# Performance work log

Measured on AMD Instinct MI355X. Metric: run time of the kernel, lower is better.

The kernel has to match this reference:

```python
import jax, jax.numpy as jnp
import numpy as np

RSD = 9   # robot_state_dim
HSD = 5   # human_state_dim (human feature slice width = HSD+1 = 6)
XD = 32   # X_dim
NEG = -9e15


def _lin(x, w, b):
    return x @ w + b


def _gat(X, adj, w0, b0, w1, b1):
    # X: [B,N,F]; pairwise concat feature (i,j) = [X_i, X_j] -> [B,N,N,2F]
    B, N, F = X.shape
    Xi = jnp.broadcast_to(X[:, :, None, :], (B, N, N, F))
    Xj = jnp.broadcast_to(X[:, None, :, :], (B, N, N, F))
    pair = jnp.concatenate([Xi, Xj], axis=-1)              # [B,N,N,2F]
    h = jax.nn.relu(_lin(pair, w0, b0))                    # [B,N,N,2F]
    A = _lin(h, w1, b1)[..., 0]                            # [B,N,N]
    e = jnp.where(A > 0, A, 0.04 * A)                      # LeakyReLU(0.04)
    att = jax.nn.softmax(jnp.where(adj > 0, e, NEG), axis=2)
    return jnp.einsum('bij,bjf->bif', att, X)


def setup_inputs() -> dict:
    key = jax.random.key(0)
    ks = jax.random.split(key, 32)
    s = 0.05
    d = {
        'state': jax.random.normal(ks[0], (512, 50, 15), jnp.float32),
        'dropout': 0,
        # w_r: Linear(9,64) ReLU Linear(64,32) ReLU
        'wr_w0': jax.random.normal(ks[1], (RSD, 64)) * s, 'wr_b0': jnp.zeros((64,)),
        'wr_w1': jax.random.normal(ks[2], (64, XD)) * s, 'wr_b1': jnp.zeros((XD,)),
        # w_h: Linear(6,64) ReLU Linear(64,32) ReLU
        'wh_w0': jax.random.normal(ks[3], (HSD + 1, 64)) * s, 'wh_b0': jnp.zeros((64,)),
        'wh_w1': jax.random.normal(ks[4], (64, XD)) * s, 'wh_b1': jnp.zeros((XD,)),
        # gat0 w_a: Linear(64,64) ReLU Linear(64,1)
        'g0_w0': jax.random.normal(ks[5], (2 * XD, 2 * XD)) * s, 'g0_b0': jnp.zeros((2 * XD,)),
        'g0_w1': jax.random.normal(ks[6], (2 * XD, 1)) * s, 'g0_b1': jnp.zeros((1,)),
        # gat1 w_a
        'g1_w0': jax.random.normal(ks[7], (2 * XD, 2 * XD)) * s, 'g1_b0': jnp.zeros((2 * XD,)),
        'g1_w1': jax.random.normal(ks[8], (2 * XD, 1)) * s, 'g1_b1': jnp.zeros((1,)),
        # value_net: Linear(32,150) ReLU Linear(150,100) ReLU Linear(100,1) ReLU
        'v_w0': jax.random.normal(ks[9], (XD, 150)) * s, 'v_b0': jnp.zeros((150,)),
        'v_w1': jax.random.normal(ks[10], (150, 100)) * s, 'v_b1': jnp.zeros((100,)),
        'v_w2': jax.random.normal(ks[11], (100, 1)) * s, 'v_b2': jnp.zeros((1,)),
    }
    return d


def reference(state, dropout, wr_w0, wr_b0, wr_w1, wr_b1, wh_w0, wh_b0, wh_w1, wh_b1,
              g0_w0, g0_b0, g0_w1, g0_b1, g1_w0, g1_b0, g1_w1, g1_b1,
              v_w0, v_b0, v_w1, v_b1, v_w2, v_b2):
    B, N, _ = state.shape
    robot = state[:, 0, :RSD]                               # [B,9]
    humans = state[:, :, RSD:]                              # [B,N,6]
    r_emb = jax.nn.relu(_lin(jax.nn.relu(_lin(robot, wr_w0, wr_b0)), wr_w1, wr_b1))[:, None, :]
    h_emb = jax.nn.relu(_lin(jax.nn.relu(_lin(humans, wh_w0, wh_b0)), wh_w1, wh_b1))
    X = jnp.concatenate([r_emb, h_emb], axis=1)             # [B,N+1,32]
    Num = N + 1
    adj = jnp.ones((Num, Num), state.dtype).at[1:, 0].set(0.0)
    adj = jnp.broadcast_to(adj[None], (B, Num, Num))
    H1 = _gat(X, adj, g0_w0, g0_b0, g0_w1, g0_b1)
    H2 = _gat(H1, adj, g1_w0, g1_b0, g1_w1, g1_b1)
    output = H1 + H2 + X                                    # skip_connection=True
    o = output[:, 0, :]
    o = jax.nn.relu(_lin(o, v_w0, v_b0))
    o = jax.nn.relu(_lin(o, v_w1, v_b1))
    o = jax.nn.relu(_lin(o, v_w2, v_b2))                    # last_relu=True
    return o
```

## Files before the change

kernel.cpp:

```cpp
#include <hip/hip_runtime.h>
#include <hip/hip_bf16.h>


typedef float f4 __attribute__((ext_vector_type(4)));
typedef const float* cfp;

__device__ __forceinline__ f4 fma4(float s, f4 v, f4 a) { return a + s * v; }
__device__ __forceinline__ f4 max4(f4 a, f4 b) {
  f4 r;
#pragma unroll
  for (int i = 0; i < 4; ++i) r[i] = fmaxf(a[i], b[i]);
  return r;
}

#define NN 51
#define HID 64
#define XD 32
#define XS 9
#define ES 52

__global__ __launch_bounds__(256)
void value_net_kernel(cfp state,
                      cfp wr_w0, cfp wr_b0, cfp wr_w1, cfp wr_b1,
                      cfp wh_w0, cfp wh_b0, cfp wh_w1, cfp wh_b1,
                      cfp g0_w0, cfp g0_b0, cfp g0_w1, cfp g0_b1,
                      cfp g1_w0, cfp g1_b0, cfp g1_w1, cfp g1_b1,
                      cfp v_w0, cfp v_b0, cfp v_w1, cfp v_b1,
                      cfp v_w2, cfp v_b2,
                      float* out)
{
  __shared__ f4 sX4[52 * XS];
  __shared__ f4 sH14[52 * XS];
  __shared__ f4 sU4[52 * 17];
  __shared__ f4 sV4[52 * 17];
  __shared__ f4 sWE4[1024];
  __shared__ f4 sB04[16];
  __shared__ f4 sW14[16];
  __shared__ float sRH[64];
  __shared__ float sO[32];
  __shared__ float sM1[152];
  __shared__ float sM2[104];

  float* sX  = (float*)sX4;
  float* sH1 = (float*)sH14;
  float* sE  = (float*)sWE4;
  float* sHH = (float*)sU4;
  const f4* sWh4 = (const f4*)sV4;

  const int tid = threadIdx.x;
  const int b = blockIdx.x;
  cfp st = state + b * 750;

  const float gb0 = g0_b1[0];
  const float gb1 = g1_b1[0];

  {
    const f4* g0w04 = (const f4*)g0_w0;
    for (int i = tid; i < 1024; i += 256) sWE4[i] = g0w04[i];
    const f4* whw14 = (const f4*)wh_w1;
    f4* sWh4w = (f4*)sV4;
    for (int i = tid; i < 512; i += 256) sWh4w[i] = whw14[i];
  }
  if (tid < HID) {
    ((float*)sB04)[tid] = g0_b0[tid];
    ((float*)sW14)[tid] = g0_w1[tid];
    float a = wr_b0[tid];
#pragma unroll
    for (int k = 0; k < 9; ++k) a = fmaf(st[k], wr_w0[k * HID + tid], a);
    sRH[tid] = fmaxf(a, 0.f);
  }
  if (tid < XS) { sX4[51 * XS + tid] = (f4){0,0,0,0}; sH14[51 * XS + tid] = (f4){0,0,0,0}; }
  for (int idx = tid; idx < 50 * HID; idx += 256) {
    int i = idx >> 6, t = idx & 63;
    cfp hp = st + i * 15 + 9;
    float a = wh_b0[t];
#pragma unroll
    for (int k = 0; k < 6; ++k) a = fmaf(hp[k], wh_w0[k * HID + t], a);
    sHH[i * 68 + t] = fmaxf(a, 0.f);
  }
  __syncthreads();

  if (tid < XD) {
    float a = wr_b1[tid];
#pragma unroll 8
    for (int t = 0; t < HID; ++t) a = fmaf(sRH[t], wr_w1[t * XD + tid], a);
    sX[tid] = fmaxf(a, 0.f);
  }
  if (tid < 200) {
    int ip = tid >> 3, fg = tid & 7;
    f4 a0 = { wh_b1[fg * 4 + 0], wh_b1[fg * 4 + 1],
              wh_b1[fg * 4 + 2], wh_b1[fg * 4 + 3] };
    f4 a1 = a0;
    const f4* h0 = sU4 + ip * 17;
    const f4* h1 = sU4 + (ip + 25) * 17;
#pragma unroll 4
    for (int tg = 0; tg < 16; ++tg) {
      f4 ha = h0[tg], hb = h1[tg];
#pragma unroll
      for (int e = 0; e < 4; ++e) {
        f4 w = sWh4[(tg * 4 + e) * 8 + fg];
        a0 = fma4(ha[e], w, a0);
        a1 = fma4(hb[e], w, a1);
      }
    }
    f4 z = {0,0,0,0};
    sX4[(1 + ip) * XS + fg] = max4(a0, z);
    sX4[(26 + ip) * XS + fg] = max4(a1, z);
  }
  __syncthreads();

  if (tid < 208) {
    int ip = tid >> 4, tg = tid & 15;
    f4 au[4] = {{0,0,0,0},{0,0,0,0},{0,0,0,0},{0,0,0,0}};
    f4 av[4] = {{0,0,0,0},{0,0,0,0},{0,0,0,0},{0,0,0,0}};
#pragma unroll 2
    for (int kg = 0; kg < 8; ++kg) {
      f4 x0 = sX4[ip * XS + kg];
      f4 x1 = sX4[(ip + 13) * XS + kg];
      f4 x2 = sX4[(ip + 26) * XS + kg];
      f4 x3 = sX4[(ip + 39) * XS + kg];
#pragma unroll
      for (int e = 0; e < 4; ++e) {
        int k = kg * 4 + e;
        f4 wU = sWE4[k * 16 + tg];
        f4 wV = sWE4[(k + 32) * 16 + tg];
        au[0] = fma4(x0[e], wU, au[0]); av[0] = fma4(x0[e], wV, av[0]);
        au[1] = fma4(x1[e], wU, au[1]); av[1] = fma4(x1[e], wV, av[1]);
        au[2] = fma4(x2[e], wU, au[2]); av[2] = fma4(x2[e], wV, av[2]);
        au[3] = fma4(x3[e], wU, au[3]); av[3] = fma4(x3[e], wV, av[3]);
      }
    }
    f4 b0v = sB04[tg];
#pragma unroll
    for (int r = 0; r < 4; ++r) {
      int row = ip + 13 * r;
      sU4[row * 17 + tg] = au[r] + b0v;
      sV4[row * 17 + tg] = av[r];
    }
  }
  __syncthreads();

  if (tid < 169) {
    int it = tid / 13, jt = tid - (tid / 13) * 13;
    const f4* U0 = sU4 + it * 17;
    const f4* V0 = sV4 + jt * 17;
    f4 acc[4][4] = {};
    const f4 z = {0,0,0,0};
#pragma unroll 2
    for (int g = 0; g < 16; ++g) {
      f4 uu[4] = {U0[g], U0[221 + g], U0[442 + g], U0[663 + g]};
      f4 vv[4] = {V0[g], V0[221 + g], V0[442 + g], V0[663 + g]};
      f4 w = sW14[g];
#pragma unroll
      for (int r = 0; r < 4; ++r)
#pragma unroll
        for (int cc = 0; cc < 4; ++cc)
          acc[r][cc] += max4(uu[r] + vv[cc], z) * w;
    }
#pragma unroll
    for (int r = 0; r < 4; ++r) {
      int i = it + 13 * r;
      if (i < NN) {
#pragma unroll
        for (int cc = 0; cc < 4; ++cc) {
          int j = jt + 13 * cc;
          if (j < NN) {
            f4 A4 = acc[r][cc];
            float A = (A4[0] + A4[1]) + (A4[2] + A4[3]) + gb0;
            float e = A > 0.f ? A : 0.04f * A;
            sE[i * ES + j] = (j == 0 && i > 0) ? -1e30f : e;
          }
        }
      }
    }
  }
  __syncthreads();

  {
    int lane = tid & 63, w = tid >> 6;
    for (int r = w; r < NN; r += 4) {
      float* row = sE + r * ES;
      float e = (lane < NN) ? row[lane] : -3.0e38f;
      float m = e;
#pragma unroll
      for (int o = 32; o; o >>= 1) m = fmaxf(m, __shfl_xor(m, o, 64));
      float p = (lane < NN) ? __expf(e - m) : 0.f;
      float s = p;
#pragma unroll
      for (int o = 32; o; o >>= 1) s += __shfl_xor(s, o, 64);
      if (lane < NN) row[lane] = p / s;
      else if (lane == NN) row[lane] = 0.f;
    }
  }
  __syncthreads();

  if (tid < 104) {
    int ip = tid >> 3, q = tid & 7;
    const f4* a0 = (const f4*)(sE + ip * ES);
    const f4* a1 = (const f4*)(sE + (ip + 13) * ES);
    const f4* a2 = (const f4*)(sE + (ip + 26) * ES);
    const f4* a3 = (const f4*)(sE + (ip + 39) * ES);
    f4 b0 = {0,0,0,0}, b1 = {0,0,0,0}, b2 = {0,0,0,0}, b3 = {0,0,0,0};
    for (int jg = 0; jg < 13; ++jg) {
      f4 t0 = a0[jg], t1 = a1[jg], t2 = a2[jg], t3 = a3[jg];
#pragma unroll
      for (int e = 0; e < 4; ++e) {
        f4 x = sX4[(jg * 4 + e) * XS + q];
        b0 = fma4(t0[e], x, b0);
        b1 = fma4(t1[e], x, b1);
        b2 = fma4(t2[e], x, b2);
        b3 = fma4(t3[e], x, b3);
      }
    }
    sH14[ip * XS + q] = b0;
    sH14[(ip + 13) * XS + q] = b1;
    sH14[(ip + 26) * XS + q] = b2;
    sH14[(ip + 39) * XS + q] = b3;
  } else if (tid < 232) {
    int t = tid - 104;
    const f4* g1w = (const f4*)g1_w0;
#pragma unroll
    for (int i = 0; i < 4; ++i) sU4[t + 128 * i] = g1w[512 + t + 128 * i];
  } else if (tid < 248) {
    sB04[tid - 232] = ((const f4*)g1_b0)[tid - 232];
  } else {
    int t = tid - 248;
    sW14[t] = ((const f4*)g1_w1)[t];
    sW14[t + 8] = ((const f4*)g1_w1)[t + 8];
  }
  __syncthreads();

  if (tid < 208) {
    int jp = tid >> 4, tg = tid & 15;
    f4 av[4] = {{0,0,0,0},{0,0,0,0},{0,0,0,0},{0,0,0,0}};
#pragma unroll 2
    for (int kg = 0; kg < 8; ++kg) {
      f4 h0 = sH14[jp * XS + kg];
      f4 h1 = sH14[(jp + 13) * XS + kg];
      f4 h2 = sH14[(jp + 26) * XS + kg];
      f4 h3 = sH14[(jp + 39) * XS + kg];
#pragma unroll
      for (int e = 0; e < 4; ++e) {
        f4 wV = sU4[(kg * 4 + e) * 16 + tg];
        av[0] = fma4(h0[e], wV, av[0]);
        av[1] = fma4(h1[e], wV, av[1]);
        av[2] = fma4(h2[e], wV, av[2]);
        av[3] = fma4(h3[e], wV, av[3]);
      }
    }
#pragma unroll
    for (int r = 0; r < 4; ++r) sV4[(jp + 13 * r) * 17 + tg] = av[r];
  } else if (tid < 224) {
    int tg = tid - 208;
    const f4* w0g = (const f4*)g1_w0;
    f4 au = {0,0,0,0};
#pragma unroll 2
    for (int kg = 0; kg < 8; ++kg) {
      f4 h = sH14[kg];
#pragma unroll
      for (int e = 0; e < 4; ++e) au = fma4(h[e], w0g[(kg * 4 + e) * 16 + tg], au);
    }
    sU4[512 + tg] = au + sB04[tg];
  }
  __syncthreads();

  if (tid < 64) {
    int j = tid;
    float e = -3.0e38f;
    if (j < NN) {
      f4 acc4 = {0,0,0,0};
#pragma unroll 4
      for (int g = 0; g < 16; ++g) {
        f4 u = sU4[512 + g];
        f4 v = sV4[j * 17 + g];
        f4 w = sW14[g];
        f4 z = {0,0,0,0};
        acc4 += max4(u + v, z) * w;
      }
      float acc = (acc4[0] + acc4[1]) + (acc4[2] + acc4[3]) + gb1;
      e = acc > 0.f ? acc : 0.04f * acc;
    }
    float m = e;
#pragma unroll
    for (int o = 32; o; o >>= 1) m = fmaxf(m, __shfl_xor(m, o, 64));
    float p = (j < NN) ? __expf(e - m) : 0.f;
    float s = p;
#pragma unroll
    for (int o = 32; o; o >>= 1) s += __shfl_xor(s, o, 64);
    if (j < NN) sE[j] = p / s;
  }
  __syncthreads();

  if (tid < XD) {
    float a = 0.f;
    for (int j = 0; j < NN; ++j) a = fmaf(sE[j], sH1[j * 36 + tid], a);
    sO[tid] = a + sH1[tid] + sX[tid];
  }
  __syncthreads();

  if (tid < 150) {
    float a = v_b0[tid];
#pragma unroll 8
    for (int k = 0; k < 32; ++k) a = fmaf(sO[k], v_w0[k * 150 + tid], a);
    sM1[tid] = fmaxf(a, 0.f);
  }
  __syncthreads();
  if (tid < 250) {
    int kp = tid / 50, t2 = tid % 50;
    const float2* w = (const float2*)v_w1;
    float2 acc = {0.f, 0.f};
    for (int k = kp * 30; k < kp * 30 + 30; ++k) {
      float2 ww = w[k * 50 + t2];
      float xv = sM1[k];
      acc.x = fmaf(xv, ww.x, acc.x);
      acc.y = fmaf(xv, ww.y, acc.y);
    }
    ((float2*)(sE + 768 + kp * 100))[t2] = acc;
  }
  __syncthreads();
  if (tid < 100) {
    float a = v_b1[tid];
#pragma unroll
    for (int kp = 0; kp < 5; ++kp) a += sE[768 + kp * 100 + tid];
    sM2[tid] = fmaxf(a, 0.f);
  }
  __syncthreads();
  if (tid < 64) {
    float a = sM2[tid] * v_w2[tid];
    if (tid < 36) a = fmaf(sM2[tid + 64], v_w2[tid + 64], a);
#pragma unroll
    for (int o = 32; o; o >>= 1) a += __shfl_xor(a, o, 64);
    if (tid == 0) out[b] = fmaxf(a + v_b2[0], 0.f);
  }
}

extern "C" void kernel_launch(void* const* d_in, const int* in_sizes, int n_in,
                              void* d_out, int out_size, void* d_ws, size_t ws_size,
                              hipStream_t stream) {
  cfp state = (cfp)d_in[0];
  cfp wr_w0 = (cfp)d_in[2],  cfp_wr_b0 = (cfp)d_in[3];
  cfp wr_w1 = (cfp)d_in[4],  wr_b1 = (cfp)d_in[5];
  cfp wh_w0 = (cfp)d_in[6],  wh_b0 = (cfp)d_in[7];
  cfp wh_w1 = (cfp)d_in[8],  wh_b1 = (cfp)d_in[9];
  cfp g0_w0 = (cfp)d_in[10], g0_b0 = (cfp)d_in[11];
  cfp g0_w1 = (cfp)d_in[12], g0_b1 = (cfp)d_in[13];
  cfp g1_w0 = (cfp)d_in[14], g1_b0 = (cfp)d_in[15];
  cfp g1_w1 = (cfp)d_in[16], g1_b1 = (cfp)d_in[17];
  cfp v_w0  = (cfp)d_in[18], v_b0  = (cfp)d_in[19];
  cfp v_w1  = (cfp)d_in[20], v_b1  = (cfp)d_in[21];
  cfp v_w2  = (cfp)d_in[22], v_b2  = (cfp)d_in[23];
  float* out = (float*)d_out;

  const int B = in_sizes[0] / 750;
  hipLaunchKernelGGL(value_net_kernel, dim3(B), dim3(256), 0, stream,
                     state,
                     wr_w0, cfp_wr_b0, wr_w1, wr_b1,
                     wh_w0, wh_b0, wh_w1, wh_b1,
                     g0_w0, g0_b0, g0_w1, g0_b1,
                     g1_w0, g1_b0, g1_w1, g1_b1,
                     v_w0, v_b0, v_w1, v_b1, v_w2, v_b2,
                     out);
}
```

Measured before the change: 137.3 us.

## Double block to 512 threads and retile GAT phases to 3x3 register tiles

The kernel launches 512 threads per block instead of 256. The pairwise attention score phase is retiled from 13x13 threads with 4x4 register tiles to 17x17 threads with 3x3 tiles, and the U/V projections, aggregation, softmax rows and value-net reduction are spread across more threads. The robot embedding's second layer moves onto otherwise idle threads so one barrier can be dropped. The aim is shorter per-block latency and less serial work per thread. The cost is more waves per block and more idle lanes in some phases, which may reduce how many blocks fit on each CU.

New measurement: 130.6 us. 1.05x faster.

```diff
diff --git a/kernel.cpp b/kernel.cpp
--- a/kernel.cpp
+++ b/kernel.cpp
@@ -19,7 +19,7 @@
 #define XS 9
 #define ES 52
 
-__global__ __launch_bounds__(256)
+__global__ __launch_bounds__(512, 4)
 void value_net_kernel(cfp state,
                       cfp wr_w0, cfp wr_b0, cfp wr_w1, cfp wr_b1,
                       cfp wh_w0, cfp wh_b0, cfp wh_w1, cfp wh_b1,
@@ -56,10 +56,10 @@
 
   {
     const f4* g0w04 = (const f4*)g0_w0;
-    for (int i = tid; i < 1024; i += 256) sWE4[i] = g0w04[i];
+    for (int i = tid; i < 1024; i += 512) sWE4[i] = g0w04[i];
     const f4* whw14 = (const f4*)wh_w1;
     f4* sWh4w = (f4*)sV4;
-    for (int i = tid; i < 512; i += 256) sWh4w[i] = whw14[i];
+    if (tid < 512) sWh4w[tid] = whw14[tid];
   }
   if (tid < HID) {
     ((float*)sB04)[tid] = g0_b0[tid];
@@ -69,8 +69,8 @@
     for (int k = 0; k < 9; ++k) a = fmaf(st[k], wr_w0[k * HID + tid], a);
     sRH[tid] = fmaxf(a, 0.f);
   }
-  if (tid < XS) { sX4[51 * XS + tid] = (f4){0,0,0,0}; sH14[51 * XS + tid] = (f4){0,0,0,0}; }
-  for (int idx = tid; idx < 50 * HID; idx += 256) {
+  if (tid >= 64 && tid < 64 + XS) sX4[51 * XS + (tid - 64)] = (f4){0,0,0,0};
+  for (int idx = tid; idx < 50 * HID; idx += 512) {
     int i = idx >> 6, t = idx & 63;
     cfp hp = st + i * 15 + 9;
     float a = wh_b0[t];
@@ -80,12 +80,6 @@
   }
   __syncthreads();
 
-  if (tid < XD) {
-    float a = wr_b1[tid];
-#pragma unroll 8
-    for (int t = 0; t < HID; ++t) a = fmaf(sRH[t], wr_w1[t * XD + tid], a);
-    sX[tid] = fmaxf(a, 0.f);
-  }
   if (tid < 200) {
     int ip = tid >> 3, fg = tid & 7;
     f4 a0 = { wh_b1[fg * 4 + 0], wh_b1[fg * 4 + 1],
@@ -106,19 +100,24 @@
     f4 z = {0,0,0,0};
     sX4[(1 + ip) * XS + fg] = max4(a0, z);
     sX4[(26 + ip) * XS + fg] = max4(a1, z);
-  }
-  __syncthreads();
-
-  if (tid < 208) {
+  } else if (tid >= 448 && tid < 448 + XD) {
+    int t = tid - 448;
+    float a = wr_b1[t];
+#pragma unroll 8
+    for (int k = 0; k < HID; ++k) a = fmaf(sRH[k], wr_w1[k * XD + t], a);
+    sX[t] = fmaxf(a, 0.f);
+  }
+  __syncthreads();
+
+  if (tid < 272) {
     int ip = tid >> 4, tg = tid & 15;
-    f4 au[4] = {{0,0,0,0},{0,0,0,0},{0,0,0,0},{0,0,0,0}};
-    f4 av[4] = {{0,0,0,0},{0,0,0,0},{0,0,0,0},{0,0,0,0}};
+    f4 au[3] = {{0,0,0,0},{0,0,0,0},{0,0,0,0}};
+    f4 av[3] = {{0,0,0,0},{0,0,0,0},{0,0,0,0}};
 #pragma unroll 2
     for (int kg = 0; kg < 8; ++kg) {
       f4 x0 = sX4[ip * XS + kg];
-      f4 x1 = sX4[(ip + 13) * XS + kg];
-      f4 x2 = sX4[(ip + 26) * XS + kg];
-      f4 x3 = sX4[(ip + 39) * XS + kg];
+      f4 x1 = sX4[(ip + 17) * XS + kg];
+      f4 x2 = sX4[(ip + 34) * XS + kg];
 #pragma unroll
       for (int e = 0; e < 4; ++e) {
         int k = kg * 4 + e;
@@ -127,50 +126,45 @@
         au[0] = fma4(x0[e], wU, au[0]); av[0] = fma4(x0[e], wV, av[0]);
         au[1] = fma4(x1[e], wU, au[1]); av[1] = fma4(x1[e], wV, av[1]);
         au[2] = fma4(x2[e], wU, au[2]); av[2] = fma4(x2[e], wV, av[2]);
-        au[3] = fma4(x3[e], wU, au[3]); av[3] = fma4(x3[e], wV, av[3]);
       }
     }
     f4 b0v = sB04[tg];
 #pragma unroll
-    for (int r = 0; r < 4; ++r) {
-      int row = ip + 13 * r;
+    for (int r = 0; r < 3; ++r) {
+      int row = ip + 17 * r;
       sU4[row * 17 + tg] = au[r] + b0v;
       sV4[row * 17 + tg] = av[r];
     }
   }
   __syncthreads();
 
-  if (tid < 169) {
-    int it = tid / 13, jt = tid - (tid / 13) * 13;
+  if (tid < 289) {
+    int it = tid / 17, jt = tid - (tid / 17) * 17;
     const f4* U0 = sU4 + it * 17;
     const f4* V0 = sV4 + jt * 17;
-    f4 acc[4][4] = {};
+    f4 acc[3][3] = {};
     const f4 z = {0,0,0,0};
-#pragma unroll 2
+#pragma unroll 4
     for (int g = 0; g < 16; ++g) {
-      f4 uu[4] = {U0[g], U0[221 + g], U0[442 + g], U0[663 + g]};
-      f4 vv[4] = {V0[g], V0[221 + g], V0[442 + g], V0[663 + g]};
+      f4 uu[3] = {U0[g], U0[289 + g], U0[578 + g]};
+      f4 vv[3] = {V0[g], V0[289 + g], V0[578 + g]};
       f4 w = sW14[g];
 #pragma unroll
-      for (int r = 0; r < 4; ++r)
-#pragma unroll
-        for (int cc = 0; cc < 4; ++cc)
+      for (int r = 0; r < 3; ++r)
+#pragma unroll
+        for (int cc = 0; cc < 3; ++cc)
           acc[r][cc] += max4(uu[r] + vv[cc], z) * w;
     }
 #pragma unroll
-    for (int r = 0; r < 4; ++r) {
-      int i = it + 13 * r;
-      if (i < NN) {
-#pragma unroll
-        for (int cc = 0; cc < 4; ++cc) {
-          int j = jt + 13 * cc;
-          if (j < NN) {
-            f4 A4 = acc[r][cc];
-            float A = (A4[0] + A4[1]) + (A4[2] + A4[3]) + gb0;
-            float e = A > 0.f ? A : 0.04f * A;
-            sE[i * ES + j] = (j == 0 && i > 0) ? -1e30f : e;
-          }
-        }
+    for (int r = 0; r < 3; ++r) {
+      int i = it + 17 * r;
+#pragma unroll
+      for (int cc = 0; cc < 3; ++cc) {
+        int j = jt + 17 * cc;
+        f4 A4 = acc[r][cc];
+        float A = (A4[0] + A4[1]) + (A4[2] + A4[3]) + gb0;
+        float e = A > 0.f ? A : 0.04f * A;
+        sE[i * ES + j] = (j == 0 && i > 0) ? -1e30f : e;
       }
     }
   }
@@ -178,7 +172,7 @@
 
   {
     int lane = tid & 63, w = tid >> 6;
-    for (int r = w; r < NN; r += 4) {
+    for (int r = w; r < NN; r += 8) {
       float* row = sE + r * ES;
       float e = (lane < NN) ? row[lane] : -3.0e38f;
       float m = e;
@@ -194,64 +188,54 @@
   }
   __syncthreads();
 
-  if (tid < 104) {
+  if (tid < 208) {
     int ip = tid >> 3, q = tid & 7;
     const f4* a0 = (const f4*)(sE + ip * ES);
-    const f4* a1 = (const f4*)(sE + (ip + 13) * ES);
-    const f4* a2 = (const f4*)(sE + (ip + 26) * ES);
-    const f4* a3 = (const f4*)(sE + (ip + 39) * ES);
-    f4 b0 = {0,0,0,0}, b1 = {0,0,0,0}, b2 = {0,0,0,0}, b3 = {0,0,0,0};
+    const f4* a1 = (const f4*)(sE + (ip + 26) * ES);
+    f4 b0 = {0,0,0,0}, b1 = {0,0,0,0};
     for (int jg = 0; jg < 13; ++jg) {
-      f4 t0 = a0[jg], t1 = a1[jg], t2 = a2[jg], t3 = a3[jg];
+      f4 t0 = a0[jg], t1 = a1[jg];
 #pragma unroll
       for (int e = 0; e < 4; ++e) {
         f4 x = sX4[(jg * 4 + e) * XS + q];
         b0 = fma4(t0[e], x, b0);
         b1 = fma4(t1[e], x, b1);
-        b2 = fma4(t2[e], x, b2);
-        b3 = fma4(t3[e], x, b3);
       }
     }
     sH14[ip * XS + q] = b0;
-    sH14[(ip + 13) * XS + q] = b1;
-    sH14[(ip + 26) * XS + q] = b2;
-    sH14[(ip + 39) * XS + q] = b3;
-  } else if (tid < 232) {
-    int t = tid - 104;
+    sH14[(ip + 26) * XS + q] = b1;
+  } else if (tid >= 384) {
+    int t = tid - 384;
     const f4* g1w = (const f4*)g1_w0;
 #pragma unroll
     for (int i = 0; i < 4; ++i) sU4[t + 128 * i] = g1w[512 + t + 128 * i];
-  } else if (tid < 248) {
-    sB04[tid - 232] = ((const f4*)g1_b0)[tid - 232];
-  } else {
-    int t = tid - 248;
-    sW14[t] = ((const f4*)g1_w1)[t];
-    sW14[t + 8] = ((const f4*)g1_w1)[t + 8];
-  }
-  __syncthreads();
-
-  if (tid < 208) {
+  } else if (tid >= 352 && tid < 368) {
+    sB04[tid - 352] = ((const f4*)g1_b0)[tid - 352];
+  } else if (tid >= 368 && tid < 384) {
+    sW14[tid - 368] = ((const f4*)g1_w1)[tid - 368];
+  }
+  __syncthreads();
+
+  if (tid < 272) {
     int jp = tid >> 4, tg = tid & 15;
-    f4 av[4] = {{0,0,0,0},{0,0,0,0},{0,0,0,0},{0,0,0,0}};
+    f4 av[3] = {{0,0,0,0},{0,0,0,0},{0,0,0,0}};
 #pragma unroll 2
     for (int kg = 0; kg < 8; ++kg) {
       f4 h0 = sH14[jp * XS + kg];
-      f4 h1 = sH14[(jp + 13) * XS + kg];
-      f4 h2 = sH14[(jp + 26) * XS + kg];
-      f4 h3 = sH14[(jp + 39) * XS + kg];
+      f4 h1 = sH14[(jp + 17) * XS + kg];
+      f4 h2 = sH14[(jp + 34) * XS + kg];
 #pragma unroll
       for (int e = 0; e < 4; ++e) {
         f4 wV = sU4[(kg * 4 + e) * 16 + tg];
         av[0] = fma4(h0[e], wV, av[0]);
         av[1] = fma4(h1[e], wV, av[1]);
         av[2] = fma4(h2[e], wV, av[2]);
-        av[3] = fma4(h3[e], wV, av[3]);
-      }
-    }
-#pragma unroll
-    for (int r = 0; r < 4; ++r) sV4[(jp + 13 * r) * 17 + tg] = av[r];
-  } else if (tid < 224) {
-    int tg = tid - 208;
+      }
+    }
+#pragma unroll
+    for (int r = 0; r < 3; ++r) sV4[(jp + 17 * r) * 17 + tg] = av[r];
+  } else if (tid < 288) {
+    int tg = tid - 272;
     const f4* w0g = (const f4*)g1_w0;
     f4 au = {0,0,0,0};
 #pragma unroll 2
@@ -305,11 +289,11 @@
     sM1[tid] = fmaxf(a, 0.f);
   }
   __syncthreads();
-  if (tid < 250) {
+  if (tid < 500) {
     int kp = tid / 50, t2 = tid % 50;
     const float2* w = (const float2*)v_w1;
     float2 acc = {0.f, 0.f};
-    for (int k = kp * 30; k < kp * 30 + 30; ++k) {
+    for (int k = kp * 15; k < kp * 15 + 15; ++k) {
       float2 ww = w[k * 50 + t2];
       float xv = sM1[k];
       acc.x = fmaf(xv, ww.x, acc.x);
@@ -321,7 +305,7 @@
   if (tid < 100) {
     float a = v_b1[tid];
 #pragma unroll
-    for (int kp = 0; kp < 5; ++kp) a += sE[768 + kp * 100 + tid];
+    for (int kp = 0; kp < 10; ++kp) a += sE[768 + kp * 100 + tid];
     sM2[tid] = fmaxf(a, 0.f);
   }
   __syncthreads();
@@ -338,7 +322,7 @@
                               void* d_out, int out_size, void* d_ws, size_t ws_size,
                               hipStream_t stream) {
   cfp state = (cfp)d_in[0];
-  cfp wr_w0 = (cfp)d_in[2],  cfp_wr_b0 = (cfp)d_in[3];
+  cfp wr_w0 = (cfp)d_in[2],  wr_b0 = (cfp)d_in[3];
   cfp wr_w1 = (cfp)d_in[4],  wr_b1 = (cfp)d_in[5];
   cfp wh_w0 = (cfp)d_in[6],  wh_b0 = (cfp)d_in[7];
   cfp wh_w1 = (cfp)d_in[8],  wh_b1 = (cfp)d_in[9];
@@ -352,9 +336,9 @@
   float* out = (float*)d_out;
 
   const int B = in_sizes[0] / 750;
-  hipLaunchKernelGGL(value_net_kernel, dim3(B), dim3(256), 0, stream,
+  hipLaunchKernelGGL(value_net_kernel, dim3(B), dim3(512), 0, stream,
                      state,
-                     wr_w0, cfp_wr_b0, wr_w1, wr_b1,
+                     wr_w0, wr_b0, wr_w1, wr_b1,
                      wh_w0, wh_b0, wh_w1, wh_b1,
                      g0_w0, g0_b0, g0_w1, g0_b1,
                      g1_w0, g1_b0, g1_w1, g1_b1,
```

## Double block size to 512 threads and redistribute per-stage work across threads

Applied to the files above, without the earlier changes.

Launches 512 threads per batch block instead of 256 and reassigns stage work across the larger thread set. The human-embedding stage now has fewer threads each computing four rows, the robot embedding runs on otherwise idle threads, and the softmax rows and value-net partial sums are spread over more warps. The final softmax and the aggregation are merged into one phase, and the value-net hidden reduction is folded into the last dot product, which removes two barriers. Risks include more idle threads per barrier, higher per-block register and occupancy pressure from the launch bounds, and reading g0_w1 from global memory inside the pairwise loop.

Result: faster. 130.5 us (-5.0%).

```diff
diff --git a/kernel.cpp b/kernel.cpp
--- a/kernel.cpp
+++ b/kernel.cpp
@@ -19,7 +19,7 @@
 #define XS 9
 #define ES 52
 
-__global__ __launch_bounds__(256)
+__global__ __launch_bounds__(512, 4)
 void value_net_kernel(cfp state,
                       cfp wr_w0, cfp wr_b0, cfp wr_w1, cfp wr_b1,
                       cfp wh_w0, cfp wh_b0, cfp wh_w1, cfp wh_b1,
@@ -39,7 +39,6 @@
   __shared__ float sRH[64];
   __shared__ float sO[32];
   __shared__ float sM1[152];
-  __shared__ float sM2[104];
 
   float* sX  = (float*)sX4;
   float* sH1 = (float*)sH14;
@@ -56,21 +55,21 @@
 
   {
     const f4* g0w04 = (const f4*)g0_w0;
-    for (int i = tid; i < 1024; i += 256) sWE4[i] = g0w04[i];
+    for (int i = tid; i < 1024; i += 512) sWE4[i] = g0w04[i];
     const f4* whw14 = (const f4*)wh_w1;
     f4* sWh4w = (f4*)sV4;
-    for (int i = tid; i < 512; i += 256) sWh4w[i] = whw14[i];
+    if (tid < 512) sWh4w[tid] = whw14[tid];
   }
   if (tid < HID) {
     ((float*)sB04)[tid] = g0_b0[tid];
-    ((float*)sW14)[tid] = g0_w1[tid];
     float a = wr_b0[tid];
 #pragma unroll
     for (int k = 0; k < 9; ++k) a = fmaf(st[k], wr_w0[k * HID + tid], a);
     sRH[tid] = fmaxf(a, 0.f);
   }
-  if (tid < XS) { sX4[51 * XS + tid] = (f4){0,0,0,0}; sH14[51 * XS + tid] = (f4){0,0,0,0}; }
-  for (int idx = tid; idx < 50 * HID; idx += 256) {
+  if (tid >= 64 && tid < 64 + XS) sX4[51 * XS + (tid - 64)] = (f4){0,0,0,0};
+  if (tid >= 96 && tid < 130) sU4[850 + (tid - 96)] = (f4){0,0,0,0};
+  for (int idx = tid; idx < 50 * HID; idx += 512) {
     int i = idx >> 6, t = idx & 63;
     cfp hp = st + i * 15 + 9;
     float a = wh_b0[t];
@@ -80,32 +79,37 @@
   }
   __syncthreads();
 
-  if (tid < XD) {
-    float a = wr_b1[tid];
-#pragma unroll 8
-    for (int t = 0; t < HID; ++t) a = fmaf(sRH[t], wr_w1[t * XD + tid], a);
-    sX[tid] = fmaxf(a, 0.f);
-  }
-  if (tid < 200) {
+  if (tid < 104) {
     int ip = tid >> 3, fg = tid & 7;
     f4 a0 = { wh_b1[fg * 4 + 0], wh_b1[fg * 4 + 1],
               wh_b1[fg * 4 + 2], wh_b1[fg * 4 + 3] };
-    f4 a1 = a0;
+    f4 a1 = a0, a2 = a0, a3 = a0;
     const f4* h0 = sU4 + ip * 17;
-    const f4* h1 = sU4 + (ip + 25) * 17;
 #pragma unroll 4
     for (int tg = 0; tg < 16; ++tg) {
-      f4 ha = h0[tg], hb = h1[tg];
+      f4 ha = h0[tg], hb = h0[13 * 17 + tg], hc = h0[26 * 17 + tg], hd = h0[39 * 17 + tg];
 #pragma unroll
       for (int e = 0; e < 4; ++e) {
         f4 w = sWh4[(tg * 4 + e) * 8 + fg];
         a0 = fma4(ha[e], w, a0);
         a1 = fma4(hb[e], w, a1);
+        a2 = fma4(hc[e], w, a2);
+        a3 = fma4(hd[e], w, a3);
       }
     }
     f4 z = {0,0,0,0};
-    sX4[(1 + ip) * XS + fg] = max4(a0, z);
-    sX4[(26 + ip) * XS + fg] = max4(a1, z);
+    f4 res[4] = {max4(a0, z), max4(a1, z), max4(a2, z), max4(a3, z)};
+#pragma unroll
+    for (int r = 0; r < 4; ++r) {
+      int hr = ip + 13 * r;
+      if (hr < 50) sX4[(1 + hr) * XS + fg] = res[r];
+    }
+  } else if (tid >= 448 && tid < 448 + XD) {
+    int t = tid - 448;
+    float a = wr_b1[t];
+#pragma unroll 8
+    for (int k = 0; k < HID; ++k) a = fmaf(sRH[k], wr_w1[k * XD + t], a);
+    sX[t] = fmaxf(a, 0.f);
   }
   __syncthreads();
 
@@ -150,7 +154,8 @@
     for (int g = 0; g < 16; ++g) {
       f4 uu[4] = {U0[g], U0[221 + g], U0[442 + g], U0[663 + g]};
       f4 vv[4] = {V0[g], V0[221 + g], V0[442 + g], V0[663 + g]};
-      f4 w = sW14[g];
+      f4 w = { g0_w1[g * 4 + 0], g0_w1[g * 4 + 1],
+               g0_w1[g * 4 + 2], g0_w1[g * 4 + 3] };
 #pragma unroll
       for (int r = 0; r < 4; ++r)
 #pragma unroll
@@ -178,7 +183,7 @@
 
   {
     int lane = tid & 63, w = tid >> 6;
-    for (int r = w; r < NN; r += 4) {
+    for (int r = w; r < NN; r += 8) {
       float* row = sE + r * ES;
       float e = (lane < NN) ? row[lane] : -3.0e38f;
       float m = e;
@@ -216,17 +221,15 @@
     sH14[(ip + 13) * XS + q] = b1;
     sH14[(ip + 26) * XS + q] = b2;
     sH14[(ip + 39) * XS + q] = b3;
-  } else if (tid < 232) {
-    int t = tid - 104;
+  } else if (tid >= 384) {
+    int t = tid - 384;
     const f4* g1w = (const f4*)g1_w0;
 #pragma unroll
     for (int i = 0; i < 4; ++i) sU4[t + 128 * i] = g1w[512 + t + 128 * i];
-  } else if (tid < 248) {
-    sB04[tid - 232] = ((const f4*)g1_b0)[tid - 232];
-  } else {
-    int t = tid - 248;
-    sW14[t] = ((const f4*)g1_w1)[t];
-    sW14[t + 8] = ((const f4*)g1_w1)[t + 8];
+  } else if (tid >= 352 && tid < 368) {
+    sB04[tid - 352] = ((const f4*)g1_b0)[tid - 352];
+  } else if (tid >= 368 && tid < 384) {
+    sW14[tid - 368] = ((const f4*)g1_w1)[tid - 368];
   }
   __syncthreads();
 
@@ -250,8 +253,8 @@
     }
 #pragma unroll
     for (int r = 0; r < 4; ++r) sV4[(jp + 13 * r) * 17 + tg] = av[r];
-  } else if (tid < 224) {
-    int tg = tid - 208;
+  } else if (tid >= 256 && tid < 272) {
+    int tg = tid - 256;
     const f4* w0g = (const f4*)g1_w0;
     f4 au = {0,0,0,0};
 #pragma unroll 2
@@ -287,14 +290,12 @@
     float s = p;
 #pragma unroll
     for (int o = 32; o; o >>= 1) s += __shfl_xor(s, o, 64);
-    if (j < NN) sE[j] = p / s;
-  }
-  __syncthreads();
-
-  if (tid < XD) {
-    float a = 0.f;
-    for (int j = 0; j < NN; ++j) a = fmaf(sE[j], sH1[j * 36 + tid], a);
-    sO[tid] = a + sH1[tid] + sX[tid];
+    sE[j] = (j < NN) ? p / s : 0.f;
+    if (tid < XD) {
+      float a = 0.f;
+      for (int jj = 0; jj < NN; ++jj) a = fmaf(sE[jj], sH1[jj * 36 + tid], a);
+      sO[tid] = a + sH1[tid] + sX[tid];
+    }
   }
   __syncthreads();
 
@@ -305,11 +306,12 @@
     sM1[tid] = fmaxf(a, 0.f);
   }
   __syncthreads();
-  if (tid < 250) {
+
+  if (tid < 500) {
     int kp = tid / 50, t2 = tid % 50;
     const float2* w = (const float2*)v_w1;
     float2 acc = {0.f, 0.f};
-    for (int k = kp * 30; k < kp * 30 + 30; ++k) {
+    for (int k = kp * 15; k < kp * 15 + 15; ++k) {
       float2 ww = w[k * 50 + t2];
       float xv = sM1[k];
       acc.x = fmaf(xv, ww.x, acc.x);
@@ -318,16 +320,18 @@
     ((float2*)(sE + 768 + kp * 100))[t2] = acc;
   }
   __syncthreads();
-  if (tid < 100) {
-    float a = v_b1[tid];
-#pragma unroll
-    for (int kp = 0; kp < 5; ++kp) a += sE[768 + kp * 100 + tid];
-    sM2[tid] = fmaxf(a, 0.f);
-  }
-  __syncthreads();
+
   if (tid < 64) {
-    float a = sM2[tid] * v_w2[tid];
-    if (tid < 36) a = fmaf(sM2[tid + 64], v_w2[tid + 64], a);
+    float a2 = v_b1[tid];
+#pragma unroll
+    for (int kp = 0; kp < 10; ++kp) a2 += sE[768 + kp * 100 + tid];
+    float a = fmaxf(a2, 0.f) * v_w2[tid];
+    if (tid < 36) {
+      float b2 = v_b1[tid + 64];
+#pragma unroll
+      for (int kp = 0; kp < 10; ++kp) b2 += sE[768 + kp * 100 + tid + 64];
+      a = fmaf(fmaxf(b2, 0.f), v_w2[tid + 64], a);
+    }
 #pragma unroll
     for (int o = 32; o; o >>= 1) a += __shfl_xor(a, o, 64);
     if (tid == 0) out[b] = fmaxf(a + v_b2[0], 0.f);
@@ -338,7 +342,7 @@
                               void* d_out, int out_size, void* d_ws, size_t ws_size,
                               hipStream_t stream) {
   cfp state = (cfp)d_in[0];
-  cfp wr_w0 = (cfp)d_in[2],  cfp_wr_b0 = (cfp)d_in[3];
+  cfp wr_w0 = (cfp)d_in[2],  wr_b0 = (cfp)d_in[3];
   cfp wr_w1 = (cfp)d_in[4],  wr_b1 = (cfp)d_in[5];
   cfp wh_w0 = (cfp)d_in[6],  wh_b0 = (cfp)d_in[7];
   cfp wh_w1 = (cfp)d_in[8],  wh_b1 = (cfp)d_in[9];
@@ -352,9 +356,9 @@
   float* out = (float*)d_out;
 
   const int B = in_sizes[0] / 750;
-  hipLaunchKernelGGL(value_net_kernel, dim3(B), dim3(256), 0, stream,
+  hipLaunchKernelGGL(value_net_kernel, dim3(B), dim3(512), 0, stream,
                      state,
-                     wr_w0, cfp_wr_b0, wr_w1, wr_b1,
+                     wr_w0, wr_b0, wr_w1, wr_b1,
                      wh_w0, wh_b0, wh_w1, wh_b1,
                      g0_w0, g0_b0, g0_w1, g0_b1,
                      g1_w0, g1_b0, g1_w1, g1_b1,
```
